# Kernel optimization log

Measured on AMD Instinct MI355X. Metric: run time of the kernel, lower is better.

The kernel has to match this reference:

```python
import jax, jax.numpy as jnp
import numpy as np

RING_SIZES = list(range(3, 27, 2))  # 3,5,...,25 -> 12 rings; (1+12)*96 = 1248
BN_EPS = 1e-5


def _box_sum(x, k):
    """Sum over k x k window (k odd), 'same' zero padding. x: [B,C,H,W].
    O(1) per pixel via summed-area table instead of dense depthwise conv."""
    p = k // 2
    H, W = x.shape[2], x.shape[3]
    xp = jnp.pad(x, ((0, 0), (0, 0), (p, p), (p, p)))
    S = jnp.cumsum(jnp.cumsum(xp, axis=2), axis=3)
    S = jnp.pad(S, ((0, 0), (0, 0), (1, 0), (1, 0)))  # leading zero row/col
    return (S[:, :, k:k + H, k:k + W] - S[:, :, :H, k:k + W]
            - S[:, :, k:k + H, :W] + S[:, :, :H, :W])


def _ring_sum(x, k):
    """Depthwise conv with a k x k ring of ones == box(k) - box(k-2)."""
    inner = x if k == 3 else _box_sum(x, k - 2)
    return _box_sum(x, k) - inner


def _bn_eval(x, gamma, beta, mean, var):
    scale = gamma / jnp.sqrt(var + BN_EPS)
    return x * scale[None, :, None, None] + (beta - mean * scale)[None, :, None, None]


def _conv1x1(x, w, b):
    # x: [B,C,H,W], w: [O,C] -> [B,O,H,W]
    return jnp.einsum('bchw,oc->bohw', x, w) + b[None, :, None, None]


def setup_inputs() -> dict:
    key = jax.random.key(0)
    ks = jax.random.split(key, 13)
    B, C, H, W = 4, 96, 128, 128
    return {
        'x': jax.random.normal(ks[0], (B, C, H, W), jnp.float32),
        'bn1_gamma': jax.random.uniform(ks[1], (1248,), jnp.float32, 0.5, 1.5),
        'bn1_beta': jax.random.normal(ks[2], (1248,), jnp.float32) * 0.1,
        'bn1_mean': jax.random.normal(ks[3], (1248,), jnp.float32),
        'bn1_var': jax.random.uniform(ks[4], (1248,), jnp.float32, 0.5, 1.5),
        'conv1_w': jax.random.normal(ks[5], (512, 1248), jnp.float32) * (1.0 / np.sqrt(1248)),
        'conv1_b': jax.random.normal(ks[6], (512,), jnp.float32) * 0.01,
        'bn2_gamma': jax.random.uniform(ks[7], (512,), jnp.float32, 0.5, 1.5),
        'bn2_beta': jax.random.normal(ks[8], (512,), jnp.float32) * 0.1,
        'bn2_mean': jax.random.normal(ks[9], (512,), jnp.float32),
        'bn2_var': jax.random.uniform(ks[10], (512,), jnp.float32, 0.5, 1.5),
        'conv2_w': jax.random.normal(ks[11], (96, 512), jnp.float32) * (1.0 / np.sqrt(512)),
        'conv2_b': jax.random.normal(ks[12], (96,), jnp.float32) * 0.01,
    }


def reference(x, bn1_gamma, bn1_beta, bn1_mean, bn1_var, conv1_w, conv1_b,
              bn2_gamma, bn2_beta, bn2_mean, bn2_var, conv2_w, conv2_b):
    convs = [x] + [_ring_sum(x, k) for k in RING_SIZES]
    h = jnp.concatenate(convs, axis=1)  # [B, 1248, H, W]
    h = _bn_eval(h, bn1_gamma, bn1_beta, bn1_mean, bn1_var)
    h = jax.nn.relu(_conv1x1(h, conv1_w, conv1_b))
    h = _bn_eval(h, bn2_gamma, bn2_beta, bn2_mean, bn2_var)
    return _conv1x1(h, conv2_w, conv2_b)
```

## Files before the change

kernel.cpp:

```cpp
#include <hip/hip_runtime.h>
#include <hip/hip_bf16.h>
#include <cstdint>

typedef __attribute__((ext_vector_type(8))) short bf16x8;
typedef __attribute__((ext_vector_type(4))) float f32x4;

#define BN_EPS 1e-5f
#define GLOBAL_AS __attribute__((address_space(1)))
#define LDS_AS __attribute__((address_space(3)))

__device__ __forceinline__ void load_lds16(const __hip_bfloat16* g, __hip_bfloat16* l) {
  __builtin_amdgcn_global_load_lds((const GLOBAL_AS uint32_t*)g, (LDS_AS uint32_t*)l, 16, 0, 0);
}

__global__ __launch_bounds__(256) void prep1_kernel(
    const float* __restrict__ W1, const float* __restrict__ cb1,
    const float* __restrict__ g1, const float* __restrict__ be1,
    const float* __restrict__ mu1, const float* __restrict__ va1,
    __hip_bfloat16* __restrict__ V, float* __restrict__ b1e)
{
  int o = blockIdx.x;
  int t = threadIdx.x;
  const float* wrow = W1 + (size_t)o * 1248;
  float acc = 0.f;
  for (int i = t; i < 1248; i += 256) {
    float s = g1[i] * rsqrtf(va1[i] + BN_EPS);
    float w = wrow[i];
    acc += w * (be1[i] - mu1[i] * s);
    float g = w * s;
    float gn = 0.f;
    if (i < 1152) {
      float sn = g1[i + 96] * rsqrtf(va1[i + 96] + BN_EPS);
      gn = wrow[i + 96] * sn;
    }
    V[(size_t)o * 1248 + i] = __float2bfloat16(g - gn);
  }
  for (int d = 32; d > 0; d >>= 1) acc += __shfl_down(acc, d);
  __shared__ float red[4];
  int lane = t & 63, wv = t >> 6;
  if (lane == 0) red[wv] = acc;
  __syncthreads();
  if (t == 0) b1e[o] = cb1[o] + red[0] + red[1] + red[2] + red[3];
}

__global__ __launch_bounds__(256) void prep2_kernel(
    const float* __restrict__ W2, const float* __restrict__ cb2,
    const float* __restrict__ g2, const float* __restrict__ be2,
    const float* __restrict__ mu2, const float* __restrict__ va2,
    __hip_bfloat16* __restrict__ W2e, float* __restrict__ b2e)
{
  int o = blockIdx.x;
  int t = threadIdx.x;
  const float* wrow = W2 + (size_t)o * 512;
  float acc = 0.f;
  for (int j = t; j < 512; j += 256) {
    float s = g2[j] * rsqrtf(va2[j] + BN_EPS);
    float wv = wrow[j];
    acc += wv * (be2[j] - mu2[j] * s);
    W2e[(size_t)o * 512 + j] = __float2bfloat16(wv * s);
  }
  for (int d = 32; d > 0; d >>= 1) acc += __shfl_down(acc, d);
  __shared__ float red[4];
  int lane = t & 63, wv2 = t >> 6;
  if (lane == 0) red[wv2] = acc;
  __syncthreads();
  if (t == 0) b2e[o] = cb2[o] + red[0] + red[1] + red[2] + red[3];
}

__global__ __launch_bounds__(128) void sat_kernel(
    const float* __restrict__ x, float* __restrict__ SAT)
{
  int plane = blockIdx.x;
  const float* xp = x + (size_t)plane * 16384;
  __shared__ float tile[16384];
  int t = threadIdx.x;
  for (int i = t; i < 16384; i += 128) {
    int r = i >> 7, c = i & 127;
    tile[r * 128 + (c ^ (r & 31))] = xp[i];
  }
  __syncthreads();
  {
    float run = 0.f;
    int r = t;
    for (int c = 0; c < 128; ++c) {
      int a = r * 128 + (c ^ (r & 31));
      run += tile[a];
      tile[a] = run;
    }
  }
  __syncthreads();
  float* Sg = SAT + (size_t)plane * 17028;
  Sg[t] = 0.f;
  if (t < 4) Sg[128 + t] = 0.f;
  Sg[(t + 1) * 132] = 0.f;
  float run = 0.f;
  for (int r = 0; r < 128; ++r) {
    run += tile[r * 128 + (t ^ (r & 31))];
    Sg[(r + 1) * 132 + t + 1] = run;
  }
}

__global__ __launch_bounds__(256) void feat_kernel(
    const float* __restrict__ SAT, __hip_bfloat16* __restrict__ Hmat)
{
  int blk = blockIdx.x;
  int xcd = blk & 7;
  int inner = blk >> 3;
  int bL = xcd >> 1;
  int yh = xcd & 1;
  int ch = inner & 1;
  int y  = yh * 64 + (inner >> 1);
  int c0 = ch * 48;
  int t = threadIdx.x;
  int tx = t & 127;
  int tc = t >> 7;

  __shared__ __align__(16) float E[48 * 132];
  __shared__ __align__(16) __hip_bfloat16 stage[48 * 129];

  const float* Sb = SAT + (size_t)(bL * 96 + c0) * 17028;
  size_t rowbase = ((size_t)bL * 16384 + (size_t)y * 128) * 1248;

  for (int j = 0; j < 13; ++j) {
    int y1 = (y - j < 0) ? 0 : (y - j);
    int y2 = ((y + j > 127) ? 127 : (y + j)) + 1;
    for (int idx = t; idx < 1584; idx += 256) {
      int cl = idx / 33;
      int ck = idx - cl * 33;
      const float* bp = Sb + (size_t)cl * 17028 + ck * 4;
      float4 a = *(const float4*)(bp + y2 * 132);
      float4 b = *(const float4*)(bp + y1 * 132);
      float* e = E + cl * 132 + ck * 4;
      e[0] = a.x - b.x; e[1] = a.y - b.y; e[2] = a.z - b.z; e[3] = a.w - b.w;
    }
    __syncthreads();
    int x1 = (tx - j < 0) ? 0 : (tx - j);
    int x2 = ((tx + j > 127) ? 127 : (tx + j)) + 1;
#pragma unroll
    for (int cc = 0; cc < 24; ++cc) {
      int cl = tc * 24 + cc;
      float v = E[cl * 132 + x2] - E[cl * 132 + x1];
      stage[cl * 129 + tx] = __float2bfloat16(v);
    }
    __syncthreads();
#pragma unroll
    for (int it = 0; it < 3; ++it) {
      int q = it * 256 + t;
      int px = q / 6;
      int chk = q - px * 6;
      union { uint4 u; __hip_bfloat16 h[8]; } v;
#pragma unroll
      for (int i = 0; i < 8; ++i)
        v.h[i] = stage[(chk * 8 + i) * 129 + px];
      *(uint4*)(Hmat + rowbase + (size_t)px * 1248 + j * 96 + c0 + chk * 8) = v.u;
    }
    __syncthreads();
  }
}

__global__ __launch_bounds__(256) void gemm1_kernel(
    const __hip_bfloat16* __restrict__ A,
    const __hip_bfloat16* __restrict__ Bv,
    const float* __restrict__ b1e,
    __hip_bfloat16* __restrict__ Y1)
{
  const int K = 1248;
  int linear = blockIdx.x;
  int xcd = linear & 7;
  int slot = linear >> 3;
  int mtiles_per_xcd = (int)(gridDim.x >> 5);
  int ntile = slot & 3;
  int mtile = xcd * mtiles_per_xcd + (slot >> 2);
  int m0 = mtile * 128;
  int n0 = ntile * 128;
  int t = threadIdx.x;
  int lane = t & 63, wv = t >> 6;
  int wm = wv & 1, wn = wv >> 1;
  int lr = lane & 15, quad = lane >> 4;

  __shared__ __align__(16) __hip_bfloat16 As[128 * 32];
  __shared__ __align__(16) __hip_bfloat16 Bs[128 * 32];

  int srow = lane >> 2;
  int scol = (lane & 3) * 8;
  const __hip_bfloat16* gA0 = A + (size_t)(m0 + wv * 16 + srow) * K + scol;
  const __hip_bfloat16* gA1 = A + (size_t)(m0 + (wv + 4) * 16 + srow) * K + scol;
  const __hip_bfloat16* gB0 = Bv + (size_t)(n0 + wv * 16 + srow) * K + scol;
  const __hip_bfloat16* gB1 = Bv + (size_t)(n0 + (wv + 4) * 16 + srow) * K + scol;
  __hip_bfloat16* lA0 = As + (wv * 16) * 32;
  __hip_bfloat16* lA1 = As + ((wv + 4) * 16) * 32;
  __hip_bfloat16* lB0 = Bs + (wv * 16) * 32;
  __hip_bfloat16* lB1 = Bs + ((wv + 4) * 16) * 32;

  f32x4 acc[4][4];
#pragma unroll
  for (int i = 0; i < 4; ++i)
#pragma unroll
    for (int jj = 0; jj < 4; ++jj) acc[i][jj] = (f32x4){0.f, 0.f, 0.f, 0.f};

  for (int k0 = 0; k0 < K; k0 += 32) {
    __syncthreads();
    load_lds16(gA0 + k0, lA0);
    load_lds16(gA1 + k0, lA1);
    load_lds16(gB0 + k0, lB0);
    load_lds16(gB1 + k0, lB1);
    __syncthreads();

    bf16x8 af[4], bfr[4];
#pragma unroll
    for (int i = 0; i < 4; ++i)
      af[i] = *(const bf16x8*)(As + (wm * 64 + i * 16 + lr) * 32 + quad * 8);
#pragma unroll
    for (int jj = 0; jj < 4; ++jj)
      bfr[jj] = *(const bf16x8*)(Bs + (wn * 64 + jj * 16 + lr) * 32 + quad * 8);
#pragma unroll
    for (int i = 0; i < 4; ++i)
#pragma unroll
      for (int jj = 0; jj < 4; ++jj)
        acc[i][jj] = __builtin_amdgcn_mfma_f32_16x16x32_bf16(af[i], bfr[jj], acc[i][jj], 0, 0, 0);
  }

#pragma unroll
  for (int jj = 0; jj < 4; ++jj) {
    int n = n0 + wn * 64 + jj * 16 + lr;
    float bias = b1e[n];
#pragma unroll
    for (int i = 0; i < 4; ++i) {
      int mbase = m0 + wm * 64 + i * 16 + quad * 4;
#pragma unroll
      for (int r = 0; r < 4; ++r) {
        float z = acc[i][jj][r] + bias;
        z = z > 0.f ? z : 0.f;
        Y1[(size_t)(mbase + r) * 512 + n] = __float2bfloat16(z);
      }
    }
  }
}

__global__ __launch_bounds__(256) void gemm2_kernel(
    const __hip_bfloat16* __restrict__ Y1,
    const __hip_bfloat16* __restrict__ W2e,
    const float* __restrict__ b2e,
    float* __restrict__ out, int b0)
{
  int lane = threadIdx.x & 63, wv = threadIdx.x >> 6;
  int lr = lane & 15, quad = lane >> 4;
  int pw = blockIdx.x * 256 + wv * 64;

  f32x4 acc[6][4];
#pragma unroll
  for (int im = 0; im < 6; ++im)
#pragma unroll
    for (int jn = 0; jn < 4; ++jn) acc[im][jn] = (f32x4){0.f, 0.f, 0.f, 0.f};

  for (int k0 = 0; k0 < 512; k0 += 32) {
    bf16x8 bfrag[4], afrag[6];
#pragma unroll
    for (int jn = 0; jn < 4; ++jn)
      bfrag[jn] = *(const bf16x8*)(Y1 + (size_t)(pw + jn * 16 + lr) * 512 + k0 + quad * 8);
#pragma unroll
    for (int im = 0; im < 6; ++im)
      afrag[im] = *(const bf16x8*)(W2e + (size_t)(im * 16 + lr) * 512 + k0 + quad * 8);
#pragma unroll
    for (int im = 0; im < 6; ++im)
#pragma unroll
      for (int jn = 0; jn < 4; ++jn)
        acc[im][jn] = __builtin_amdgcn_mfma_f32_16x16x32_bf16(afrag[im], bfrag[jn], acc[im][jn], 0, 0, 0);
  }

#pragma unroll
  for (int im = 0; im < 6; ++im) {
#pragma unroll
    for (int r = 0; r < 4; ++r) {
      int o2 = im * 16 + quad * 4 + r;
      float bias = b2e[o2];
#pragma unroll
      for (int jn = 0; jn < 4; ++jn) {
        int p = pw + jn * 16 + lr;
        out[((size_t)(b0 + (p >> 14)) * 96 + o2) * 16384 + (p & 16383)] =
            acc[im][jn][r] + bias;
      }
    }
  }
}

extern "C" void kernel_launch(void* const* d_in, const int* in_sizes, int n_in,
                              void* d_out, int out_size, void* d_ws, size_t ws_size,
                              hipStream_t stream)
{
  const float* x   = (const float*)d_in[0];
  const float* g1  = (const float*)d_in[1];
  const float* be1 = (const float*)d_in[2];
  const float* mu1 = (const float*)d_in[3];
  const float* va1 = (const float*)d_in[4];
  const float* W1  = (const float*)d_in[5];
  const float* cb1 = (const float*)d_in[6];
  const float* g2  = (const float*)d_in[7];
  const float* be2 = (const float*)d_in[8];
  const float* mu2 = (const float*)d_in[9];
  const float* va2 = (const float*)d_in[10];
  const float* W2  = (const float*)d_in[11];
  const float* cb2 = (const float*)d_in[12];
  float* out = (float*)d_out;

  char* w = (char*)d_ws;
  __hip_bfloat16* V   = (__hip_bfloat16*)w; w += (size_t)512 * 1248 * 2;
  __hip_bfloat16* W2e = (__hip_bfloat16*)w; w += (size_t)96 * 512 * 2;
  float* b1e = (float*)w; w += 2048;
  float* b2e = (float*)w; w += 512;
  size_t fixed = (size_t)(w - (char*)d_ws);

  const size_t satB = (size_t)96 * 17028 * 4;
  const size_t hB   = (size_t)16384 * 1248 * 2;
  const size_t yB   = (size_t)16384 * 512 * 2;
  int nb = (ws_size >= fixed + 4 * (satB + hB + yB) + 4096) ? 4 : 1;

  float* SAT = (float*)w; w += (size_t)nb * satB;
  w = (char*)(((uintptr_t)w + 255) & ~(uintptr_t)255);
  __hip_bfloat16* Hm = (__hip_bfloat16*)w; w += (size_t)nb * hB;
  __hip_bfloat16* Y1 = (__hip_bfloat16*)w;

  prep1_kernel<<<512, 256, 0, stream>>>(W1, cb1, g1, be1, mu1, va1, V, b1e);
  prep2_kernel<<<96, 256, 0, stream>>>(W2, cb2, g2, be2, mu2, va2, W2e, b2e);

  for (int b0 = 0; b0 < 4; b0 += nb) {
    sat_kernel<<<nb * 96, 128, 0, stream>>>(x + (size_t)b0 * 96 * 16384, SAT);
    feat_kernel<<<nb * 256, 256, 0, stream>>>(SAT, Hm);
    gemm1_kernel<<<nb * 512, 256, 0, stream>>>(Hm, V, b1e, Y1);
    gemm2_kernel<<<nb * 64, 256, 0, stream>>>(Y1, W2e, b2e, out, b0);
  }
}
```

Before: 337.9 us.

## Fuse ring feature construction into first GEMM, eliminating intermediate feature matrix

Replaces the separate feature-materialization kernel and GEMM1 with one kernel per image row. It builds bf16 ring-sum A tiles in LDS from the SAT and runs MFMA against V, which is loaded directly from global memory. This removes writing and re-reading the large 1248-wide feature matrix in HBM. In exchange, each block re-reads all of V without LDS staging, uses more barriers per K step, and launches fewer, larger blocks.

New measurement: 317.6 us. 6.0% less time.

```diff
diff --git a/kernel.cpp b/kernel.cpp
--- a/kernel.cpp
+++ b/kernel.cpp
@@ -6,12 +6,6 @@
 typedef __attribute__((ext_vector_type(4))) float f32x4;
 
 #define BN_EPS 1e-5f
-#define GLOBAL_AS __attribute__((address_space(1)))
-#define LDS_AS __attribute__((address_space(3)))
-
-__device__ __forceinline__ void load_lds16(const __hip_bfloat16* g, __hip_bfloat16* l) {
-  __builtin_amdgcn_global_load_lds((const GLOBAL_AS uint32_t*)g, (LDS_AS uint32_t*)l, 16, 0, 0);
-}
 
 __global__ __launch_bounds__(256) void prep1_kernel(
     const float* __restrict__ W1, const float* __restrict__ cb1,
@@ -100,138 +94,98 @@
   }
 }
 
-__global__ __launch_bounds__(256) void feat_kernel(
-    const float* __restrict__ SAT, __hip_bfloat16* __restrict__ Hmat)
-{
+__global__ __launch_bounds__(512, 2) void fused1_kernel(
+    const float* __restrict__ SAT, const __hip_bfloat16* __restrict__ V,
+    const float* __restrict__ b1e, __hip_bfloat16* __restrict__ Y1, int nb)
+{
+  __shared__ __align__(16) float E[96 * 132];
+  __shared__ __align__(16) __hip_bfloat16 As[128 * 40];
+
   int blk = blockIdx.x;
-  int xcd = blk & 7;
-  int inner = blk >> 3;
-  int bL = xcd >> 1;
-  int yh = xcd & 1;
-  int ch = inner & 1;
-  int y  = yh * 64 + (inner >> 1);
-  int c0 = ch * 48;
-  int t = threadIdx.x;
-  int tx = t & 127;
-  int tc = t >> 7;
-
-  __shared__ __align__(16) float E[48 * 132];
-  __shared__ __align__(16) __hip_bfloat16 stage[48 * 129];
-
-  const float* Sb = SAT + (size_t)(bL * 96 + c0) * 17028;
-  size_t rowbase = ((size_t)bL * 16384 + (size_t)y * 128) * 1248;
-
-  for (int j = 0; j < 13; ++j) {
+  int rows_per_xcd = (nb * 128) >> 3;
+  int r = (blk & 7) * rows_per_xcd + (blk >> 3);
+  int bL = r >> 7, y = r & 127;
+
+  int t = threadIdx.x;
+  int lane = t & 63, wv = t >> 6;
+  int lr = lane & 15, quad = lane >> 4;
+
+  const float* Sb = SAT + (size_t)bL * 96 * 17028;
+
+  int bpx = t & 127;
+  int bg = t >> 7;
+
+  f32x4 acc[8][4];
+#pragma unroll
+  for (int i = 0; i < 8; ++i)
+#pragma unroll
+    for (int jn = 0; jn < 4; ++jn) acc[i][jn] = (f32x4){0.f, 0.f, 0.f, 0.f};
+
+  auto efill = [&](int j) {
     int y1 = (y - j < 0) ? 0 : (y - j);
     int y2 = ((y + j > 127) ? 127 : (y + j)) + 1;
-    for (int idx = t; idx < 1584; idx += 256) {
+    for (int idx = t; idx < 3168; idx += 512) {
       int cl = idx / 33;
       int ck = idx - cl * 33;
       const float* bp = Sb + (size_t)cl * 17028 + ck * 4;
       float4 a = *(const float4*)(bp + y2 * 132);
       float4 b = *(const float4*)(bp + y1 * 132);
-      float* e = E + cl * 132 + ck * 4;
-      e[0] = a.x - b.x; e[1] = a.y - b.y; e[2] = a.z - b.z; e[3] = a.w - b.w;
-    }
-    __syncthreads();
-    int x1 = (tx - j < 0) ? 0 : (tx - j);
-    int x2 = ((tx + j > 127) ? 127 : (tx + j)) + 1;
-#pragma unroll
-    for (int cc = 0; cc < 24; ++cc) {
-      int cl = tc * 24 + cc;
-      float v = E[cl * 132 + x2] - E[cl * 132 + x1];
-      stage[cl * 129 + tx] = __float2bfloat16(v);
-    }
-    __syncthreads();
-#pragma unroll
-    for (int it = 0; it < 3; ++it) {
-      int q = it * 256 + t;
-      int px = q / 6;
-      int chk = q - px * 6;
-      union { uint4 u; __hip_bfloat16 h[8]; } v;
+      float4 d;
+      d.x = a.x - b.x; d.y = a.y - b.y; d.z = a.z - b.z; d.w = a.w - b.w;
+      *(float4*)(E + cl * 132 + ck * 4) = d;
+    }
+  };
+
+  int x1 = 0, x2 = 0;
+  auto build = [&](int j, int sub) {
+    const float* Eb = E + (sub * 32 + bg * 8) * 132;
+    union { bf16x8 v; __hip_bfloat16 h[8]; } pk;
+#pragma unroll
+    for (int i = 0; i < 8; ++i)
+      pk.h[i] = __float2bfloat16(Eb[i * 132 + x2] - Eb[i * 132 + x1]);
+    *(bf16x8*)(As + bpx * 40 + bg * 8) = pk.v;
+  };
+
+  efill(0);
+  __syncthreads();
+
+  for (int j = 0; j < 13; ++j) {
+    x1 = (bpx - j < 0) ? 0 : (bpx - j);
+    x2 = ((bpx + j > 127) ? 127 : (bpx + j)) + 1;
+    for (int sub = 0; sub < 3; ++sub) {
+      build(j, sub);
+      __syncthreads();
+      if (sub == 2 && j < 12) efill(j + 1);
+      bf16x8 af[8], bfr[4];
 #pragma unroll
       for (int i = 0; i < 8; ++i)
-        v.h[i] = stage[(chk * 8 + i) * 129 + px];
-      *(uint4*)(Hmat + rowbase + (size_t)px * 1248 + j * 96 + c0 + chk * 8) = v.u;
-    }
-    __syncthreads();
-  }
-}
-
-__global__ __launch_bounds__(256) void gemm1_kernel(
-    const __hip_bfloat16* __restrict__ A,
-    const __hip_bfloat16* __restrict__ Bv,
-    const float* __restrict__ b1e,
-    __hip_bfloat16* __restrict__ Y1)
-{
-  const int K = 1248;
-  int linear = blockIdx.x;
-  int xcd = linear & 7;
-  int slot = linear >> 3;
-  int mtiles_per_xcd = (int)(gridDim.x >> 5);
-  int ntile = slot & 3;
-  int mtile = xcd * mtiles_per_xcd + (slot >> 2);
-  int m0 = mtile * 128;
-  int n0 = ntile * 128;
-  int t = threadIdx.x;
-  int lane = t & 63, wv = t >> 6;
-  int wm = wv & 1, wn = wv >> 1;
-  int lr = lane & 15, quad = lane >> 4;
-
-  __shared__ __align__(16) __hip_bfloat16 As[128 * 32];
-  __shared__ __align__(16) __hip_bfloat16 Bs[128 * 32];
-
-  int srow = lane >> 2;
-  int scol = (lane & 3) * 8;
-  const __hip_bfloat16* gA0 = A + (size_t)(m0 + wv * 16 + srow) * K + scol;
-  const __hip_bfloat16* gA1 = A + (size_t)(m0 + (wv + 4) * 16 + srow) * K + scol;
-  const __hip_bfloat16* gB0 = Bv + (size_t)(n0 + wv * 16 + srow) * K + scol;
-  const __hip_bfloat16* gB1 = Bv + (size_t)(n0 + (wv + 4) * 16 + srow) * K + scol;
-  __hip_bfloat16* lA0 = As + (wv * 16) * 32;
-  __hip_bfloat16* lA1 = As + ((wv + 4) * 16) * 32;
-  __hip_bfloat16* lB0 = Bs + (wv * 16) * 32;
-  __hip_bfloat16* lB1 = Bs + ((wv + 4) * 16) * 32;
-
-  f32x4 acc[4][4];
-#pragma unroll
-  for (int i = 0; i < 4; ++i)
-#pragma unroll
-    for (int jj = 0; jj < 4; ++jj) acc[i][jj] = (f32x4){0.f, 0.f, 0.f, 0.f};
-
-  for (int k0 = 0; k0 < K; k0 += 32) {
-    __syncthreads();
-    load_lds16(gA0 + k0, lA0);
-    load_lds16(gA1 + k0, lA1);
-    load_lds16(gB0 + k0, lB0);
-    load_lds16(gB1 + k0, lB1);
-    __syncthreads();
-
-    bf16x8 af[4], bfr[4];
-#pragma unroll
-    for (int i = 0; i < 4; ++i)
-      af[i] = *(const bf16x8*)(As + (wm * 64 + i * 16 + lr) * 32 + quad * 8);
-#pragma unroll
-    for (int jj = 0; jj < 4; ++jj)
-      bfr[jj] = *(const bf16x8*)(Bs + (wn * 64 + jj * 16 + lr) * 32 + quad * 8);
-#pragma unroll
-    for (int i = 0; i < 4; ++i)
-#pragma unroll
-      for (int jj = 0; jj < 4; ++jj)
-        acc[i][jj] = __builtin_amdgcn_mfma_f32_16x16x32_bf16(af[i], bfr[jj], acc[i][jj], 0, 0, 0);
-  }
-
-#pragma unroll
-  for (int jj = 0; jj < 4; ++jj) {
-    int n = n0 + wn * 64 + jj * 16 + lr;
+        af[i] = *(const bf16x8*)(As + (i * 16 + lr) * 40 + quad * 8);
+#pragma unroll
+      for (int jn = 0; jn < 4; ++jn)
+        bfr[jn] = *(const bf16x8*)(V + (size_t)(wv * 64 + jn * 16 + lr) * 1248
+                                   + j * 96 + sub * 32 + quad * 8);
+#pragma unroll
+      for (int i = 0; i < 8; ++i)
+#pragma unroll
+        for (int jn = 0; jn < 4; ++jn)
+          acc[i][jn] = __builtin_amdgcn_mfma_f32_16x16x32_bf16(af[i], bfr[jn], acc[i][jn], 0, 0, 0);
+      __syncthreads();
+    }
+  }
+
+  size_t mrow = (size_t)bL * 16384 + (size_t)y * 128;
+#pragma unroll
+  for (int jn = 0; jn < 4; ++jn) {
+    int n = wv * 64 + jn * 16 + lr;
     float bias = b1e[n];
 #pragma unroll
-    for (int i = 0; i < 4; ++i) {
-      int mbase = m0 + wm * 64 + i * 16 + quad * 4;
-#pragma unroll
-      for (int r = 0; r < 4; ++r) {
-        float z = acc[i][jj][r] + bias;
+    for (int i = 0; i < 8; ++i) {
+      int pbase = i * 16 + quad * 4;
+#pragma unroll
+      for (int rr = 0; rr < 4; ++rr) {
+        float z = acc[i][jn][rr] + bias;
         z = z > 0.f ? z : 0.f;
-        Y1[(size_t)(mbase + r) * 512 + n] = __float2bfloat16(z);
+        Y1[(mrow + pbase + rr) * 512 + n] = __float2bfloat16(z);
       }
     }
   }
@@ -311,13 +265,11 @@
   size_t fixed = (size_t)(w - (char*)d_ws);
 
   const size_t satB = (size_t)96 * 17028 * 4;
-  const size_t hB   = (size_t)16384 * 1248 * 2;
   const size_t yB   = (size_t)16384 * 512 * 2;
-  int nb = (ws_size >= fixed + 4 * (satB + hB + yB) + 4096) ? 4 : 1;
+  int nb = (ws_size >= fixed + 4 * (satB + yB) + 4096) ? 4 : 1;
 
   float* SAT = (float*)w; w += (size_t)nb * satB;
   w = (char*)(((uintptr_t)w + 255) & ~(uintptr_t)255);
-  __hip_bfloat16* Hm = (__hip_bfloat16*)w; w += (size_t)nb * hB;
   __hip_bfloat16* Y1 = (__hip_bfloat16*)w;
 
   prep1_kernel<<<512, 256, 0, stream>>>(W1, cb1, g1, be1, mu1, va1, V, b1e);
@@ -325,8 +277,7 @@
 
   for (int b0 = 0; b0 < 4; b0 += nb) {
     sat_kernel<<<nb * 96, 128, 0, stream>>>(x + (size_t)b0 * 96 * 16384, SAT);
-    feat_kernel<<<nb * 256, 256, 0, stream>>>(SAT, Hm);
-    gemm1_kernel<<<nb * 512, 256, 0, stream>>>(Hm, V, b1e, Y1);
+    fused1_kernel<<<nb * 128, 512, 0, stream>>>(SAT, V, b1e, Y1, nb);
     gemm2_kernel<<<nb * 64, 256, 0, stream>>>(Y1, W2e, b2e, out, b0);
   }
 }
```
